# Kernel tuning notes

Hardware: AMD Instinct MI355X
Metric: run time of the kernel (lower is better)

The kernel has to match this reference:

```python
import jax, jax.numpy as jnp
import numpy as np

B, N, C, K = 8, 4096, 64, 30
EPS_BN = 1e-5
TINY = 1e-20  # guards sqrt/atan2 at the exact self-neighbor (rel == 0)


def _knn(p, k):
    xx = jnp.sum(p * p, axis=1)  # [B, N]
    pd = 2.0 * jnp.einsum('bdn,bdm->bnm', p, p) - xx[:, :, None] - xx[:, None, :]
    return jax.lax.top_k(pd, k)[1]  # [B, N, k]


def _bn(h, g, b):
    # BatchNorm1d in training mode: biased batch stats over all dims but channel (last)
    mu = jnp.mean(h, axis=(0, 1, 2), keepdims=True)
    var = jnp.var(h, axis=(0, 1, 2), keepdims=True)
    return (h - mu) * jax.lax.rsqrt(var + EPS_BN) * g + b


def _forward(x_loc, x, W1, g1, b1, W2, g2, b2, W3, g3, b3, k):
    Bsz = x.shape[0]
    idx = _knn(x_loc, k)                       # [B, N, k]
    bidx = jnp.arange(Bsz)[:, None, None]
    pts = x_loc.transpose(0, 2, 1)             # [B, N, 3]
    rel = pts[bidx, idx] - pts[:, :, None, :]  # [B, N, k, 3] neighbor - center
    xr, yr, zr = rel[..., 0], rel[..., 1], rel[..., 2]
    sxy2 = xr * xr + yr * yr
    r2 = sxy2 + zr * zr
    rho = jnp.sqrt(jnp.maximum(r2, TINY))
    sxy = jnp.sqrt(jnp.maximum(sxy2, TINY))
    deg_r = r2 < TINY
    deg_p = sxy2 < TINY
    theta = jnp.arctan2(jnp.where(deg_r, 0.0, zr), jnp.where(deg_r, 1.0, sxy))
    phi = jnp.arctan2(jnp.where(deg_p, 0.0, yr), jnp.where(deg_p, 1.0, xr))
    sph = jnp.stack([rho, theta, phi], axis=-1)            # [B, N, k, 3]
    # torch car2sph averages across the 3 spherical channels (dim=-1)
    feat = jnp.concatenate([sph, sph - jnp.mean(sph, axis=-1, keepdims=True)], axis=-1)  # [B,N,k,6]
    lrelu = lambda h: jax.nn.leaky_relu(h, 0.2)
    h = lrelu(_bn(feat @ W1.T, g1, b1))        # [B, N, k, 6]
    h = lrelu(_bn(h @ W2.T, g2, b2))           # [B, N, k, 3]
    h = lrelu(_bn(h @ W3.T, g3, b3))           # [B, N, k, 1]
    att = jax.nn.softmax(h[..., 0], axis=-1)   # [B, N, k]
    xk = x.transpose(0, 2, 1)[bidx, idx]       # [B, N, k, C]
    agg = jnp.einsum('bnkc,bnk->bnc', xk, att)
    return x + agg.transpose(0, 2, 1)          # [B, C, N]


def setup_inputs() -> dict:
    key = jax.random.key(0)
    ks = jax.random.split(key, 12)
    return {
        'x_loc': jax.random.normal(ks[0], (B, 3, N), jnp.float32),
        'x': jax.random.normal(ks[1], (B, C, N), jnp.float32),
        'W1': jax.random.normal(ks[2], (6, 6), jnp.float32) * 0.4,
        'g1': 1.0 + 0.1 * jax.random.normal(ks[3], (6,), jnp.float32),
        'b1': 0.1 * jax.random.normal(ks[4], (6,), jnp.float32),
        'W2': jax.random.normal(ks[5], (3, 6), jnp.float32) * 0.4,
        'g2': 1.0 + 0.1 * jax.random.normal(ks[6], (3,), jnp.float32),
        'b2': 0.1 * jax.random.normal(ks[7], (3,), jnp.float32),
        'W3': jax.random.normal(ks[8], (1, 3), jnp.float32) * 0.4,
        'g3': 1.0 + 0.1 * jax.random.normal(ks[9], (1,), jnp.float32),
        'b3': 0.1 * jax.random.normal(ks[10], (1,), jnp.float32),
        'k': K,
    }


def reference(x_loc, x, W1, g1, b1, W2, g2, b2, W3, g3, b3, k):
    return _forward(x_loc, x, W1, g1, b1, W2, g2, b2, W3, g3, b3, k)
```

## Files before the change

kernel.cpp:

```cpp
#include <hip/hip_runtime.h>
#include <math.h>

#define NPTS 4096
#define NB   8
#define NC   64
#define KSEL 30
#define NROWS (NB * NPTS * KSEL)
#define CNT_F 983040.0f
#define SURVZ 3840
#define P23_BLOCKS 480
#define P23_STRIDE (P23_BLOCKS * 256)

static __device__ __forceinline__ unsigned long long shfl_xor_u64(unsigned long long v, int lx) {
    int lo = __shfl_xor((int)(unsigned)(v & 0xFFFFFFFFULL), lx, 64);
    int hi = __shfl_xor((int)(unsigned)(v >> 32), lx, 64);
    return ((unsigned long long)(unsigned)hi << 32) | (unsigned)lo;
}

static __device__ __forceinline__ unsigned mbcnt64(unsigned long long m) {
    return __builtin_amdgcn_mbcnt_hi((unsigned)(m >> 32),
           __builtin_amdgcn_mbcnt_lo((unsigned)m, 0u));
}

template <int NM>
static __device__ __forceinline__ void slot_reduce(const float* __restrict__ acc,
                                                   float* __restrict__ sSum, int tid) {
    if (tid < 64) {
        float pm[NM];
#pragma unroll
        for (int m = 0; m < NM; ++m) pm[m] = acc[m * 64 + tid];
#pragma unroll
        for (int o = 32; o > 0; o >>= 1) {
#pragma unroll
            for (int m = 0; m < NM; ++m) pm[m] += __shfl_xor(pm[m], o, 64);
        }
        if (tid == 0) {
#pragma unroll
            for (int m = 0; m < NM; ++m) sSum[m] = pm[m];
        }
    }
}

static __device__ __forceinline__ void bn1_params(const float* __restrict__ sSum,
                                                  const float* __restrict__ W1,
                                                  const float* __restrict__ g1,
                                                  const float* __restrict__ b1,
                                                  float* __restrict__ sPar, int tid) {
    if (tid < 6) {
        const float invN = 1.0f / CNT_F;
        const float m0 = sSum[0] * invN, m1 = sSum[1] * invN, m2 = sSum[2] * invN;
        const float E00 = sSum[3] * invN, E01 = sSum[4] * invN, E02 = sSum[5] * invN;
        const float E11 = sSum[6] * invN, E12 = sSum[7] * invN, E22 = sSum[8] * invN;
        const float* w = W1 + tid * 6;
        const float third = (w[3] + w[4] + w[5]) * (1.0f / 3.0f);
        const float a0 = w[0] + w[3] - third;
        const float a1 = w[1] + w[4] - third;
        const float a2 = w[2] + w[5] - third;
        const float mu = a0 * m0 + a1 * m1 + a2 * m2;
        const float E2 = a0 * a0 * E00 + a1 * a1 * E11 + a2 * a2 * E22 +
                         2.0f * (a0 * a1 * E01 + a0 * a2 * E02 + a1 * a2 * E12);
        const float var = E2 - mu * mu;
        const float sc = g1[tid] / sqrtf(var + 1e-5f);
        sPar[tid] = sc;
        sPar[6 + tid] = b1[tid] - mu * sc;
    }
}

static __device__ __forceinline__ void bn2_params(const float* __restrict__ sSum,
                                                  const float* __restrict__ W2,
                                                  const float* __restrict__ g2,
                                                  const float* __restrict__ b2,
                                                  float* __restrict__ sPar, int tid) {
    if (tid < 3) {
        const float invN = 1.0f / CNT_F;
        float Eh[6];
#pragma unroll
        for (int d = 0; d < 6; ++d) Eh[d] = sSum[d] * invN;
        float M[6][6];
        int q = 6;
#pragma unroll
        for (int a2 = 0; a2 < 6; ++a2)
#pragma unroll
            for (int b2_ = a2; b2_ < 6; ++b2_) {
                const float v = sSum[q++] * invN;
                M[a2][b2_] = v; M[b2_][a2] = v;
            }
        const float* w = W2 + tid * 6;
        float mu = 0.0f;
#pragma unroll
        for (int d = 0; d < 6; ++d) mu += w[d] * Eh[d];
        float E2 = 0.0f;
#pragma unroll
        for (int a2 = 0; a2 < 6; ++a2)
#pragma unroll
            for (int b2_ = 0; b2_ < 6; ++b2_) E2 += w[a2] * w[b2_] * M[a2][b2_];
        const float var = E2 - mu * mu;
        const float sc = g2[tid] / sqrtf(var + 1e-5f);
        sPar[12 + tid] = sc;
        sPar[15 + tid] = b2[tid] - mu * sc;
    }
}

static __device__ __forceinline__ void bn3_params(const float* __restrict__ sSum,
                                                  const float* __restrict__ W3,
                                                  const float* __restrict__ g3,
                                                  const float* __restrict__ b3,
                                                  float* __restrict__ sPar, int tid) {
    if (tid == 0) {
        const float invN = 1.0f / CNT_F;
        const float Eh0 = sSum[0] * invN, Eh1 = sSum[1] * invN, Eh2 = sSum[2] * invN;
        const float M00 = sSum[3] * invN, M01 = sSum[4] * invN, M02 = sSum[5] * invN;
        const float M11 = sSum[6] * invN, M12 = sSum[7] * invN, M22 = sSum[8] * invN;
        const float w0 = W3[0], w1 = W3[1], w2 = W3[2];
        const float mu = w0 * Eh0 + w1 * Eh1 + w2 * Eh2;
        const float E2 = w0 * w0 * M00 + w1 * w1 * M11 + w2 * w2 * M22 +
                         2.0f * (w0 * w1 * M01 + w0 * w2 * M02 + w1 * w2 * M12);
        const float var = E2 - mu * mu;
        const float sc = g3[0] / sqrtf(var + 1e-5f);
        sPar[0] = sc;
        sPar[1] = b3[0] - mu * sc;
    }
}

static __device__ __forceinline__ void mlp_h1(float s0, float s1, float s2,
                                              const float* __restrict__ W1,
                                              const float* __restrict__ sPar,
                                              float* __restrict__ h1) {
    const float mean = (s0 + s1 + s2) * (1.0f / 3.0f);
    const float f[6] = {s0, s1, s2, s0 - mean, s1 - mean, s2 - mean};
#pragma unroll
    for (int c = 0; c < 6; ++c) {
        float a = 0.0f;
#pragma unroll
        for (int d = 0; d < 6; ++d) a = fmaf(W1[c * 6 + d], f[d], a);
        const float z = fmaf(a, sPar[c], sPar[6 + c]);
        h1[c] = z >= 0.0f ? z : 0.2f * z;
    }
}

static __device__ __forceinline__ void mlp_h2(const float* __restrict__ h1,
                                              const float* __restrict__ W2,
                                              const float* __restrict__ sPar,
                                              float* __restrict__ h2) {
#pragma unroll
    for (int c = 0; c < 3; ++c) {
        float a = 0.0f;
#pragma unroll
        for (int d = 0; d < 6; ++d) a = fmaf(W2[c * 6 + d], h1[d], a);
        const float z = fmaf(a, sPar[12 + c], sPar[15 + c]);
        h2[c] = z >= 0.0f ? z : 0.2f * z;
    }
}

__global__ __launch_bounds__(512, 4) void knn_k(const float* __restrict__ xloc,
                                                int* __restrict__ idx_out,
                                                float* __restrict__ sph,
                                                float* __restrict__ accM,
                                                const float* __restrict__ xg,
                                                float* __restrict__ xT) {
    __shared__ float4 pts[NPTS];
    __shared__ float msc[72];

    const int tid  = threadIdx.x;
    const int lane = tid & 63;
    const int wv   = tid >> 6;
    const int b    = blockIdx.y;
    const int n    = (blockIdx.x << 3) + wv;

    const float* xb = xloc + (size_t)b * (3 * NPTS);
    for (int i = tid; i < NPTS; i += 512) {
        const float x = xb[i], y = xb[NPTS + i], z = xb[2 * NPTS + i];
        const float xx = __fadd_rn(__fadd_rn(__fmul_rn(x, x), __fmul_rn(y, y)), __fmul_rn(z, z));
        pts[i] = make_float4(x, y, z, xx);
    }
    __syncthreads();

    const float4 q = pts[n];

    unsigned K[64];
    float lm = -3.402823466e38f;
#pragma unroll
    for (int t = 0; t < 64; ++t) {
        const float4 c = pts[lane + (t << 6)];
        const float dt = __fadd_rn(__fadd_rn(__fmul_rn(q.x, c.x), __fmul_rn(q.y, c.y)), __fmul_rn(q.z, c.z));
        const float pd = __fsub_rn(__fsub_rn(__fmul_rn(2.0f, dt), q.w), c.w);
        K[t] = __float_as_uint(pd);
        lm = fmaxf(lm, pd);
    }

    float v = lm;
#pragma unroll
    for (int k = 2; k <= 64; k <<= 1) {
#pragma unroll
        for (int j2 = k >> 1; j2 > 0; j2 >>= 1) {
            const float o = __shfl_xor(v, j2, 64);
            const bool keepmax = ((lane & j2) == 0) == ((lane & k) == 0);
            const float mx = v > o ? v : o;
            const float mn = v > o ? o : v;
            v = keepmax ? mx : mn;
        }
    }
    const float tauf = __shfl(v, 30, 64);

    __syncthreads();

    unsigned long long* surv = ((unsigned long long*)(pts + SURVZ)) + (wv << 6);
    surv[lane] = 0ULL;

    unsigned total = 0;
#pragma unroll
    for (int t = 0; t < 64; ++t) {
        const bool p = (__uint_as_float(K[t]) >= tauf);
        const unsigned long long m = __ballot(p);
        if (p) {
            const unsigned pos = total + mbcnt64(m);
            if (pos < 64u) {
                const unsigned u = K[t];
                const unsigned key = u ^ ((unsigned)((int)u >> 31) | 0x80000000u);
                const unsigned j = (unsigned)(lane + (t << 6));
                surv[pos] = ((unsigned long long)key << 32) | (unsigned)(~j);
            }
        }
        total += (unsigned)__popcll(m);
    }
    __threadfence_block();

    const int bn = (b << 12) + n;
    const size_t obase = (size_t)bn * KSEL;
    int jn = 0;

    if (total <= 64u) {
        unsigned long long s = surv[lane];
#pragma unroll
        for (int k = 2; k <= 64; k <<= 1) {
#pragma unroll
            for (int j2 = k >> 1; j2 > 0; j2 >>= 1) {
                const unsigned long long o = shfl_xor_u64(s, j2);
                const bool keepmax = ((lane & j2) == 0) == ((lane & k) == 0);
                const unsigned long long mx = s > o ? s : o;
                const unsigned long long mn = s > o ? o : s;
                s = keepmax ? mx : mn;
            }
        }
        jn = (int)(~(unsigned)s) & (NPTS - 1);
        if (lane >= KSEL) jn = 0;
    } else {
#pragma unroll
        for (int t = 0; t < 64; ++t) {
            const unsigned u = K[t];
            K[t] = u ^ ((unsigned)((int)u >> 31) | 0x80000000u);
        }
        unsigned P = 0;
        for (int bit = 31; bit >= 0; --bit) {
            const unsigned cand = P | (1u << bit);
            int c = 0;
#pragma unroll
            for (int t = 0; t < 64; ++t) c += (K[t] >= cand) ? 1 : 0;
#pragma unroll
            for (int o = 32; o > 0; o >>= 1) c += __shfl_xor(c, o, 64);
            if (c >= KSEL) P = cand;
        }
        int* sj = (int*)surv;
        int emitted = 0;
#pragma unroll
        for (int t = 0; t < 64; ++t) {
            const bool g = (K[t] > P);
            const unsigned long long m = __ballot(g);
            if (g) {
                const int pos = emitted + (int)mbcnt64(m);
                if (pos < KSEL) sj[pos] = lane + (t << 6);
            }
            emitted += (int)__popcll(m);
        }
#pragma unroll
        for (int t = 0; t < 64; ++t) {
            const bool e_ = (K[t] == P);
            const unsigned long long m = __ballot(e_);
            const int before = (int)mbcnt64(m);
            if (e_ && (emitted + before) < KSEL) sj[emitted + before] = lane + (t << 6);
            emitted += (int)__popcll(m);
        }
        __threadfence_block();
        if (lane < KSEL) jn = sj[lane];
    }

    float s0 = 0.0f, s1 = 0.0f, s2 = 0.0f;
    if (lane < KSEL) {
        idx_out[obase + lane] = jn;
        float cx, cy, cz;
        if (jn >= SURVZ) {
            cx = xb[jn]; cy = xb[NPTS + jn]; cz = xb[2 * NPTS + jn];
        } else {
            const float4 c = pts[jn];
            cx = c.x; cy = c.y; cz = c.z;
        }
        const float xr = cx - q.x, yr = cy - q.y, zr = cz - q.z;
        const float sxy2 = xr * xr + yr * yr;
        const float r2   = sxy2 + zr * zr;
        const float rho  = sqrtf(fmaxf(r2, 1e-20f));
        const float sxy  = sqrtf(fmaxf(sxy2, 1e-20f));
        const bool dr = r2 < 1e-20f;
        const bool dp = sxy2 < 1e-20f;
        const float theta = atan2f(dr ? 0.0f : zr, dr ? 1.0f : sxy);
        const float phi   = atan2f(dp ? 0.0f : yr, dp ? 1.0f : xr);
        sph[obase + lane]             = rho;
        sph[NROWS + obase + lane]     = theta;
        sph[2 * NROWS + obase + lane] = phi;
        s0 = rho; s1 = theta; s2 = phi;
    }

    float mom[9] = {s0, s1, s2, s0 * s0, s0 * s1, s0 * s2, s1 * s1, s1 * s2, s2 * s2};
#pragma unroll
    for (int o = 32; o > 0; o >>= 1) {
#pragma unroll
        for (int m = 0; m < 9; ++m) mom[m] += __shfl_xor(mom[m], o, 64);
    }
    if (lane == 0) {
#pragma unroll
        for (int m = 0; m < 9; ++m) msc[wv * 9 + m] = mom[m];
    }
    __syncthreads();
    if (tid < 9) {
        float t_ = 0.0f;
#pragma unroll
        for (int w = 0; w < 8; ++w) t_ += msc[w * 9 + tid];
        atomicAdd(&accM[tid * 64 + ((blockIdx.y * 512 + blockIdx.x) & 63)], t_);
    }

    if (blockIdx.x < 64) {
        __syncthreads();
        float* tile = (float*)pts;
        const int n0 = (int)blockIdx.x << 6;
        const int tx = tid & 63;
        const int ty = tid >> 6;
        const float* xs = xg + ((size_t)b << 18);
#pragma unroll
        for (int i = 0; i < 8; ++i) {
            const int c = (i << 3) + ty;
            tile[c * 65 + tx] = xs[((size_t)c << 12) + n0 + tx];
        }
        __syncthreads();
        float* ob = xT + ((size_t)b << 18);
#pragma unroll
        for (int i = 0; i < 8; ++i) {
            const int nl = (i << 3) + ty;
            ob[((size_t)(n0 + nl) << 6) + tx] = tile[tx * 65 + nl];
        }
    }
}

__global__ __launch_bounds__(256) void p2_k(const float* __restrict__ sph,
                                            const float* __restrict__ W1,
                                            const float* __restrict__ g1,
                                            const float* __restrict__ b1,
                                            const float* __restrict__ accM,
                                            float* __restrict__ acc2) {
    __shared__ float sSum[9];
    __shared__ float sPar[12];
    __shared__ float red[4][27];
    const int tid = threadIdx.x;
    slot_reduce<9>(accM, sSum, tid);
    __syncthreads();
    bn1_params(sSum, W1, g1, b1, sPar, tid);
    __syncthreads();

    float m27[27];
#pragma unroll
    for (int m = 0; m < 27; ++m) m27[m] = 0.0f;
#pragma unroll
    for (int s = 0; s < 8; ++s) {
        const size_t r = (size_t)blockIdx.x * 256 + tid + (size_t)s * P23_STRIDE;
        const float s0 = sph[r], s1 = sph[NROWS + r], s2 = sph[2 * NROWS + r];
        float h1[6];
        mlp_h1(s0, s1, s2, W1, sPar, h1);
        int qq = 6;
#pragma unroll
        for (int a2 = 0; a2 < 6; ++a2) {
            m27[a2] += h1[a2];
#pragma unroll
            for (int b2_ = a2; b2_ < 6; ++b2_) m27[qq++] += h1[a2] * h1[b2_];
        }
    }
#pragma unroll
    for (int o = 32; o > 0; o >>= 1) {
#pragma unroll
        for (int m = 0; m < 27; ++m) m27[m] += __shfl_xor(m27[m], o, 64);
    }
    const int lane = tid & 63, wv = tid >> 6;
    if (lane == 0) {
#pragma unroll
        for (int m = 0; m < 27; ++m) red[wv][m] = m27[m];
    }
    __syncthreads();
    if (tid < 27) {
        const float v = red[0][tid] + red[1][tid] + red[2][tid] + red[3][tid];
        atomicAdd(&acc2[tid * 64 + (blockIdx.x & 63)], v);
    }
}

__global__ __launch_bounds__(256) void p3_k(const float* __restrict__ sph,
                                            const float* __restrict__ W1,
                                            const float* __restrict__ g1,
                                            const float* __restrict__ b1,
                                            const float* __restrict__ W2,
                                            const float* __restrict__ g2,
                                            const float* __restrict__ b2,
                                            const float* __restrict__ W3,
                                            const float* __restrict__ accM,
                                            const float* __restrict__ acc2,
                                            float* __restrict__ acc3,
                                            float* __restrict__ y3) {
    __shared__ float sSum[27];
    __shared__ float sPar[18];
    __shared__ float red[4][9];
    const int tid = threadIdx.x;
    slot_reduce<9>(accM, sSum, tid);
    __syncthreads();
    bn1_params(sSum, W1, g1, b1, sPar, tid);
    __syncthreads();
    slot_reduce<27>(acc2, sSum, tid);
    __syncthreads();
    bn2_params(sSum, W2, g2, b2, sPar, tid);
    __syncthreads();

    const float w30 = W3[0], w31 = W3[1], w32 = W3[2];

    float m9[9];
#pragma unroll
    for (int m = 0; m < 9; ++m) m9[m] = 0.0f;
#pragma unroll
    for (int s = 0; s < 8; ++s) {
        const size_t r = (size_t)blockIdx.x * 256 + tid + (size_t)s * P23_STRIDE;
        const float s0 = sph[r], s1 = sph[NROWS + r], s2 = sph[2 * NROWS + r];
        float h1[6], h2[3];
        mlp_h1(s0, s1, s2, W1, sPar, h1);
        mlp_h2(h1, W2, sPar, h2);
        y3[r] = fmaf(w30, h2[0], fmaf(w31, h2[1], w32 * h2[2]));
        m9[0] += h2[0]; m9[1] += h2[1]; m9[2] += h2[2];
        m9[3] += h2[0] * h2[0]; m9[4] += h2[0] * h2[1]; m9[5] += h2[0] * h2[2];
        m9[6] += h2[1] * h2[1]; m9[7] += h2[1] * h2[2]; m9[8] += h2[2] * h2[2];
    }
#pragma unroll
    for (int o = 32; o > 0; o >>= 1) {
#pragma unroll
        for (int m = 0; m < 9; ++m) m9[m] += __shfl_xor(m9[m], o, 64);
    }
    const int lane = tid & 63, wv = tid >> 6;
    if (lane == 0) {
#pragma unroll
        for (int m = 0; m < 9; ++m) red[wv][m] = m9[m];
    }
    __syncthreads();
    if (tid < 9) {
        const float v = red[0][tid] + red[1][tid] + red[2][tid] + red[3][tid];
        atomicAdd(&acc3[tid * 64 + (blockIdx.x & 63)], v);
    }
}

__global__ __launch_bounds__(256) void p4_k(const float* __restrict__ y3,
                                            const int* __restrict__ idx,
                                            const float* __restrict__ x,
                                            const float* __restrict__ xT,
                                            const float* __restrict__ W3,
                                            const float* __restrict__ g3,
                                            const float* __restrict__ b3,
                                            const float* __restrict__ acc3,
                                            float* __restrict__ out) {
    __shared__ float sSum[9];
    __shared__ float sPar[2];
    __shared__ float agg[32][65];
    const int tid = threadIdx.x;
    slot_reduce<9>(acc3, sSum, tid);
    __syncthreads();
    bn3_params(sSum, W3, g3, b3, sPar, tid);
    __syncthreads();
    const float sc3 = sPar[0], tb3 = sPar[1];

    const int lane = tid & 63, wv = tid >> 6;
    const int b    = blockIdx.x & 7;
    const int n0   = (blockIdx.x >> 3) << 5;
    const int p0   = (b << 12) + n0;
    const float* xTb = xT + ((size_t)b << 18);
    const int g  = lane >> 4;
    const int c4 = (lane & 15) << 2;

    for (int i = 0; i < 8; ++i) {
        const int pl = (wv << 3) + i;
        const int p  = p0 + pl;
        float a = -3.4e38f;
        int jn = 0;
        if (lane < KSEL) {
            const size_t r = (size_t)p * KSEL + lane;
            const float z = fmaf(y3[r], sc3, tb3);
            a = z >= 0.0f ? z : 0.2f * z;
            jn = idx[r];
        }
        float mx = a;
#pragma unroll
        for (int o = 32; o > 0; o >>= 1) mx = fmaxf(mx, __shfl_xor(mx, o, 64));
        const float e = (lane < KSEL) ? expf(a - mx) : 0.0f;
        float se = e;
#pragma unroll
        for (int o = 32; o > 0; o >>= 1) se += __shfl_xor(se, o, 64);
        const float w = e / se;

        float ax = 0.0f, ay = 0.0f, az = 0.0f, aw = 0.0f;
#pragma unroll
        for (int r8 = 0; r8 < 8; ++r8) {
            const int t = (r8 << 2) + g;
            const int   j  = __shfl(jn, t, 64);
            const float wt = __shfl(w,  t, 64);
            const float4 v = *reinterpret_cast<const float4*>(xTb + ((size_t)j << 6) + c4);
            ax = fmaf(wt, v.x, ax); ay = fmaf(wt, v.y, ay);
            az = fmaf(wt, v.z, az); aw = fmaf(wt, v.w, aw);
        }
        ax += __shfl_xor(ax, 32, 64); ay += __shfl_xor(ay, 32, 64);
        az += __shfl_xor(az, 32, 64); aw += __shfl_xor(aw, 32, 64);
        ax += __shfl_xor(ax, 16, 64); ay += __shfl_xor(ay, 16, 64);
        az += __shfl_xor(az, 16, 64); aw += __shfl_xor(aw, 16, 64);
        if (g == 0) {
            agg[pl][c4]     = ax; agg[pl][c4 + 1] = ay;
            agg[pl][c4 + 2] = az; agg[pl][c4 + 3] = aw;
        }
    }
    __syncthreads();

    const float* xb = x + ((size_t)b << 18);
    float* ob = out + ((size_t)b << 18);
    const int nl = tid & 31, cb = tid >> 5;
#pragma unroll
    for (int i = 0; i < 8; ++i) {
        const int c = (i << 3) + cb;
        const size_t off = ((size_t)c << 12) + n0 + nl;
        ob[off] = xb[off] + agg[nl][c];
    }
}

extern "C" void kernel_launch(void* const* d_in, const int* in_sizes, int n_in,
                              void* d_out, int out_size, void* d_ws, size_t ws_size,
                              hipStream_t stream) {
    const float* x_loc = (const float*)d_in[0];
    const float* x     = (const float*)d_in[1];
    const float* W1    = (const float*)d_in[2];
    const float* g1    = (const float*)d_in[3];
    const float* b1    = (const float*)d_in[4];
    const float* W2    = (const float*)d_in[5];
    const float* g2    = (const float*)d_in[6];
    const float* b2    = (const float*)d_in[7];
    const float* W3    = (const float*)d_in[8];
    const float* g3    = (const float*)d_in[9];
    const float* b3    = (const float*)d_in[10];
    float* out = (float*)d_out;

    float* accM = (float*)d_ws;
    float* acc2 = accM + 576;
    float* acc3 = acc2 + 1728;
    float* sph  = acc3 + 576;
    int*   idx  = (int*)(sph + 3 * (size_t)NROWS);
    float* y3   = (float*)(idx + NROWS);
    float* xT   = y3 + NROWS;

    hipMemsetAsync(d_ws, 0, 11520, stream);

    knn_k<<<dim3(NPTS / 8, NB), 512, 0, stream>>>(x_loc, idx, sph, accM, x, xT);
    p2_k<<<P23_BLOCKS, 256, 0, stream>>>(sph, W1, g1, b1, accM, acc2);
    p3_k<<<P23_BLOCKS, 256, 0, stream>>>(sph, W1, g1, b1, W2, g2, b2, W3, accM, acc2, acc3, y3);
    p4_k<<<(NB * NPTS) / 32, 256, 0, stream>>>(y3, idx, x, xT, W3, g3, b3, acc3, out);
}
```

Baseline: 237.7 us.

## Pack spherical features and y3 into float4 rows and raise p2/p3 block count

Changes the per-neighbor spherical feature storage from three planar arrays plus a separate y3 array to one interleaved float4 array, with y3 written into the fourth component. p2/p3/p4 then do single 16-byte loads instead of three strided loads, and the grid grows from 480 to 1920 blocks with fewer rows per thread. The layout change adds a partial 4-byte write per row in p3, which may cost extra read-modify-write traffic on the 16-byte lines. More blocks also means more atomics into the slot accumulators.

Result: slower. 257.3 us (+8.3%).

```diff
diff --git a/kernel.cpp b/kernel.cpp
--- a/kernel.cpp
+++ b/kernel.cpp
@@ -8,7 +8,7 @@
 #define NROWS (NB * NPTS * KSEL)
 #define CNT_F 983040.0f
 #define SURVZ 3840
-#define P23_BLOCKS 480
+#define P23_BLOCKS 1920
 #define P23_STRIDE (P23_BLOCKS * 256)
 
 static __device__ __forceinline__ unsigned long long shfl_xor_u64(unsigned long long v, int lx) {
@@ -154,7 +154,7 @@
 
 __global__ __launch_bounds__(512, 4) void knn_k(const float* __restrict__ xloc,
                                                 int* __restrict__ idx_out,
-                                                float* __restrict__ sph,
+                                                float4* __restrict__ sph4,
                                                 float* __restrict__ accM,
                                                 const float* __restrict__ xg,
                                                 float* __restrict__ xT) {
@@ -303,9 +303,7 @@
         const bool dp = sxy2 < 1e-20f;
         const float theta = atan2f(dr ? 0.0f : zr, dr ? 1.0f : sxy);
         const float phi   = atan2f(dp ? 0.0f : yr, dp ? 1.0f : xr);
-        sph[obase + lane]             = rho;
-        sph[NROWS + obase + lane]     = theta;
-        sph[2 * NROWS + obase + lane] = phi;
+        sph4[obase + lane] = make_float4(rho, theta, phi, 0.0f);
         s0 = rho; s1 = theta; s2 = phi;
     }
 
@@ -349,7 +347,7 @@
     }
 }
 
-__global__ __launch_bounds__(256) void p2_k(const float* __restrict__ sph,
+__global__ __launch_bounds__(256) void p2_k(const float4* __restrict__ sph4,
                                             const float* __restrict__ W1,
                                             const float* __restrict__ g1,
                                             const float* __restrict__ b1,
@@ -368,11 +366,11 @@
 #pragma unroll
     for (int m = 0; m < 27; ++m) m27[m] = 0.0f;
 #pragma unroll
-    for (int s = 0; s < 8; ++s) {
+    for (int s = 0; s < 2; ++s) {
         const size_t r = (size_t)blockIdx.x * 256 + tid + (size_t)s * P23_STRIDE;
-        const float s0 = sph[r], s1 = sph[NROWS + r], s2 = sph[2 * NROWS + r];
+        const float4 sv = sph4[r];
         float h1[6];
-        mlp_h1(s0, s1, s2, W1, sPar, h1);
+        mlp_h1(sv.x, sv.y, sv.z, W1, sPar, h1);
         int qq = 6;
 #pragma unroll
         for (int a2 = 0; a2 < 6; ++a2) {
@@ -398,7 +396,7 @@
     }
 }
 
-__global__ __launch_bounds__(256) void p3_k(const float* __restrict__ sph,
+__global__ __launch_bounds__(256) void p3_k(float4* __restrict__ sph4,
                                             const float* __restrict__ W1,
                                             const float* __restrict__ g1,
                                             const float* __restrict__ b1,
@@ -408,8 +406,7 @@
                                             const float* __restrict__ W3,
                                             const float* __restrict__ accM,
                                             const float* __restrict__ acc2,
-                                            float* __restrict__ acc3,
-                                            float* __restrict__ y3) {
+                                            float* __restrict__ acc3) {
     __shared__ float sSum[27];
     __shared__ float sPar[18];
     __shared__ float red[4][9];
@@ -429,13 +426,13 @@
 #pragma unroll
     for (int m = 0; m < 9; ++m) m9[m] = 0.0f;
 #pragma unroll
-    for (int s = 0; s < 8; ++s) {
+    for (int s = 0; s < 2; ++s) {
         const size_t r = (size_t)blockIdx.x * 256 + tid + (size_t)s * P23_STRIDE;
-        const float s0 = sph[r], s1 = sph[NROWS + r], s2 = sph[2 * NROWS + r];
+        const float4 sv = sph4[r];
         float h1[6], h2[3];
-        mlp_h1(s0, s1, s2, W1, sPar, h1);
+        mlp_h1(sv.x, sv.y, sv.z, W1, sPar, h1);
         mlp_h2(h1, W2, sPar, h2);
-        y3[r] = fmaf(w30, h2[0], fmaf(w31, h2[1], w32 * h2[2]));
+        ((float*)(sph4 + r))[3] = fmaf(w30, h2[0], fmaf(w31, h2[1], w32 * h2[2]));
         m9[0] += h2[0]; m9[1] += h2[1]; m9[2] += h2[2];
         m9[3] += h2[0] * h2[0]; m9[4] += h2[0] * h2[1]; m9[5] += h2[0] * h2[2];
         m9[6] += h2[1] * h2[1]; m9[7] += h2[1] * h2[2]; m9[8] += h2[2] * h2[2];
@@ -457,7 +454,7 @@
     }
 }
 
-__global__ __launch_bounds__(256) void p4_k(const float* __restrict__ y3,
+__global__ __launch_bounds__(256) void p4_k(const float4* __restrict__ sph4,
                                             const int* __restrict__ idx,
                                             const float* __restrict__ x,
                                             const float* __restrict__ xT,
@@ -491,7 +488,7 @@
         int jn = 0;
         if (lane < KSEL) {
             const size_t r = (size_t)p * KSEL + lane;
-            const float z = fmaf(y3[r], sc3, tb3);
+            const float z = fmaf(((const float*)(sph4 + r))[3], sc3, tb3);
             a = z >= 0.0f ? z : 0.2f * z;
             jn = idx[r];
         }
@@ -552,18 +549,17 @@
     const float* b3    = (const float*)d_in[10];
     float* out = (float*)d_out;
 
-    float* accM = (float*)d_ws;
-    float* acc2 = accM + 576;
-    float* acc3 = acc2 + 1728;
-    float* sph  = acc3 + 576;
-    int*   idx  = (int*)(sph + 3 * (size_t)NROWS);
-    float* y3   = (float*)(idx + NROWS);
-    float* xT   = y3 + NROWS;
+    float*  accM = (float*)d_ws;
+    float*  acc2 = accM + 576;
+    float*  acc3 = acc2 + 1728;
+    float4* sph4 = (float4*)(acc3 + 576);
+    int*    idx  = (int*)(sph4 + (size_t)NROWS);
+    float*  xT   = (float*)(idx + NROWS);
 
     hipMemsetAsync(d_ws, 0, 11520, stream);
 
-    knn_k<<<dim3(NPTS / 8, NB), 512, 0, stream>>>(x_loc, idx, sph, accM, x, xT);
-    p2_k<<<P23_BLOCKS, 256, 0, stream>>>(sph, W1, g1, b1, accM, acc2);
-    p3_k<<<P23_BLOCKS, 256, 0, stream>>>(sph, W1, g1, b1, W2, g2, b2, W3, accM, acc2, acc3, y3);
-    p4_k<<<(NB * NPTS) / 32, 256, 0, stream>>>(y3, idx, x, xT, W3, g3, b3, acc3, out);
-}
+    knn_k<<<dim3(NPTS / 8, NB), 512, 0, stream>>>(x_loc, idx, sph4, accM, x, xT);
+    p2_k<<<P23_BLOCKS, 256, 0, stream>>>(sph4, W1, g1, b1, accM, acc2);
+    p3_k<<<P23_BLOCKS, 256, 0, stream>>>(sph4, W1, g1, b1, W2, g2, b2, W3, accM, acc2, acc3);
+    p4_k<<<(NB * NPTS) / 32, 256, 0, stream>>>(sph4, idx, x, xT, W3, g3, b3, acc3, out);
+}
```

## Compact kNN survivors via per-lane bitmask and prefix scan in dedicated LDS

Applied to the files above, without the earlier changes.

Replaces the 64-iteration ballot/mbcnt survivor compaction with per-lane survivor bitmasks, a wave-wide prefix scan, and a loop over set bits that recomputes distances from LDS. Moves the survivor buffer into its own shared array, so the __syncthreads before reuse of the points region goes away and neighbour coordinates always come from LDS instead of falling back to global memory. This adds 4 KB of shared memory per block and a divergent per-lane loop whose length depends on how many survivors each lane holds.

After: 222.7 us. -6.3%, faster.

```diff
diff --git a/kernel.cpp b/kernel.cpp
--- a/kernel.cpp
+++ b/kernel.cpp
@@ -7,7 +7,6 @@
 #define KSEL 30
 #define NROWS (NB * NPTS * KSEL)
 #define CNT_F 983040.0f
-#define SURVZ 3840
 #define P23_BLOCKS 480
 #define P23_STRIDE (P23_BLOCKS * 256)
 
@@ -15,11 +14,6 @@
     int lo = __shfl_xor((int)(unsigned)(v & 0xFFFFFFFFULL), lx, 64);
     int hi = __shfl_xor((int)(unsigned)(v >> 32), lx, 64);
     return ((unsigned long long)(unsigned)hi << 32) | (unsigned)lo;
-}
-
-static __device__ __forceinline__ unsigned mbcnt64(unsigned long long m) {
-    return __builtin_amdgcn_mbcnt_hi((unsigned)(m >> 32),
-           __builtin_amdgcn_mbcnt_lo((unsigned)m, 0u));
 }
 
 template <int NM>
@@ -159,6 +153,7 @@
                                                 const float* __restrict__ xg,
                                                 float* __restrict__ xT) {
     __shared__ float4 pts[NPTS];
+    __shared__ unsigned long long survA[512];
     __shared__ float msc[72];
 
     const int tid  = threadIdx.x;
@@ -202,26 +197,41 @@
     }
     const float tauf = __shfl(v, 30, 64);
 
-    __syncthreads();
-
-    unsigned long long* surv = ((unsigned long long*)(pts + SURVZ)) + (wv << 6);
+    unsigned long long* surv = survA + (wv << 6);
     surv[lane] = 0ULL;
 
-    unsigned total = 0;
-#pragma unroll
-    for (int t = 0; t < 64; ++t) {
-        const bool p = (__uint_as_float(K[t]) >= tauf);
-        const unsigned long long m = __ballot(p);
-        if (p) {
-            const unsigned pos = total + mbcnt64(m);
-            if (pos < 64u) {
-                const unsigned u = K[t];
-                const unsigned key = u ^ ((unsigned)((int)u >> 31) | 0x80000000u);
-                const unsigned j = (unsigned)(lane + (t << 6));
-                surv[pos] = ((unsigned long long)key << 32) | (unsigned)(~j);
-            }
-        }
-        total += (unsigned)__popcll(m);
+    unsigned mLo = 0u, mHi = 0u;
+#pragma unroll
+    for (int t = 0; t < 32; ++t)
+        if (__uint_as_float(K[t]) >= tauf) mLo |= (1u << t);
+#pragma unroll
+    for (int t = 32; t < 64; ++t)
+        if (__uint_as_float(K[t]) >= tauf) mHi |= (1u << (t - 32));
+    const int cnt = __popc(mLo) + __popc(mHi);
+
+    int inc = cnt;
+#pragma unroll
+    for (int o = 1; o < 64; o <<= 1) {
+        const int pv = __shfl_up(inc, o, 64);
+        if (lane >= o) inc += pv;
+    }
+    const unsigned total = (unsigned)__shfl(inc, 63, 64);
+    int pos = inc - cnt;
+
+    unsigned long long mask = ((unsigned long long)mHi << 32) | (unsigned long long)mLo;
+    if (pos >= 64) mask = 0ULL;
+    while (mask) {
+        const int t = (int)(__ffsll((unsigned long long)mask) - 1);
+        mask &= mask - 1ULL;
+        const float4 c = pts[lane + (t << 6)];
+        const float dt = __fadd_rn(__fadd_rn(__fmul_rn(q.x, c.x), __fmul_rn(q.y, c.y)), __fmul_rn(q.z, c.z));
+        const float pd = __fsub_rn(__fsub_rn(__fmul_rn(2.0f, dt), q.w), c.w);
+        const unsigned u = __float_as_uint(pd);
+        const unsigned key = u ^ ((unsigned)((int)u >> 31) | 0x80000000u);
+        const unsigned j = (unsigned)(lane + (t << 6));
+        surv[pos] = ((unsigned long long)key << 32) | (unsigned)(~j);
+        ++pos;
+        if (pos >= 64) break;
     }
     __threadfence_block();
 
@@ -267,8 +277,8 @@
             const bool g = (K[t] > P);
             const unsigned long long m = __ballot(g);
             if (g) {
-                const int pos = emitted + (int)mbcnt64(m);
-                if (pos < KSEL) sj[pos] = lane + (t << 6);
+                const int p_ = emitted + (int)__popcll(m & ((1ULL << lane) - 1ULL));
+                if (p_ < KSEL) sj[p_] = lane + (t << 6);
             }
             emitted += (int)__popcll(m);
         }
@@ -276,7 +286,7 @@
         for (int t = 0; t < 64; ++t) {
             const bool e_ = (K[t] == P);
             const unsigned long long m = __ballot(e_);
-            const int before = (int)mbcnt64(m);
+            const int before = (int)__popcll(m & ((1ULL << lane) - 1ULL));
             if (e_ && (emitted + before) < KSEL) sj[emitted + before] = lane + (t << 6);
             emitted += (int)__popcll(m);
         }
@@ -287,14 +297,8 @@
     float s0 = 0.0f, s1 = 0.0f, s2 = 0.0f;
     if (lane < KSEL) {
         idx_out[obase + lane] = jn;
-        float cx, cy, cz;
-        if (jn >= SURVZ) {
-            cx = xb[jn]; cy = xb[NPTS + jn]; cz = xb[2 * NPTS + jn];
-        } else {
-            const float4 c = pts[jn];
-            cx = c.x; cy = c.y; cz = c.z;
-        }
-        const float xr = cx - q.x, yr = cy - q.y, zr = cz - q.z;
+        const float4 c = pts[jn];
+        const float xr = c.x - q.x, yr = c.y - q.y, zr = c.z - q.z;
         const float sxy2 = xr * xr + yr * yr;
         const float r2   = sxy2 + zr * zr;
         const float rho  = sqrtf(fmaxf(r2, 1e-20f));
```
